# Performance work log

Measured on AMD Instinct MI355X. Metric: run time of the kernel, lower is better.

## Reference

```python
import jax, jax.numpy as jnp
import numpy as np

D_MODEL, D_STATE, D_CONV, D_INNER, DT_RANK, K = 96, 16, 3, 192, 6, 4
B, H, W = 1, 64, 64


def setup_inputs() -> dict:
    key = jax.random.key(0)
    ks = jax.random.split(key, 10)
    x = jax.random.normal(ks[0], (B, H, W, D_MODEL), jnp.float32)
    in_proj_w = jax.random.normal(ks[1], (2 * D_INNER, D_MODEL), jnp.float32) * 0.02
    conv_w = jax.random.normal(ks[2], (D_INNER, 1, D_CONV, D_CONV), jnp.float32) * 0.1
    conv_b = jnp.zeros((D_INNER,), jnp.float32)
    x_proj_w = jax.random.normal(ks[3], (K, DT_RANK + 2 * D_STATE, D_INNER), jnp.float32) * 0.02
    dt_std = DT_RANK ** -0.5
    dt_w = jax.random.uniform(ks[4], (K, D_INNER, DT_RANK), jnp.float32, -dt_std, dt_std)
    # dt bias init: inv-softplus of dt ~ logUniform(1e-3, 1e-1)
    u = jax.random.uniform(ks[5], (K, D_INNER), jnp.float32)
    dt = jnp.exp(u * (np.log(0.1) - np.log(0.001)) + np.log(0.001)).clip(1e-4)
    dt_b = dt + jnp.log(-jnp.expm1(-dt))
    A_logs = jnp.log(jnp.broadcast_to(jnp.arange(1, D_STATE + 1, dtype=jnp.float32), (K * D_INNER, D_STATE)))
    Ds = jnp.ones((K * D_INNER,), jnp.float32)
    ln_g = jnp.ones((D_INNER,), jnp.float32)
    ln_b = jnp.zeros((D_INNER,), jnp.float32)
    out_proj_w = jax.random.normal(ks[6], (D_MODEL, D_INNER), jnp.float32) * 0.02
    return dict(x=x, in_proj_w=in_proj_w, conv_w=conv_w, conv_b=conv_b, x_proj_w=x_proj_w,
                dt_w=dt_w, dt_b=dt_b, A_logs=A_logs, Ds=Ds, ln_g=ln_g, ln_b=ln_b,
                out_proj_w=out_proj_w)


def _ss2d(x, in_proj_w, conv_w, conv_b, x_proj_w, dt_w, dt_b, A_logs, Ds, ln_g, ln_b, out_proj_w):
    b, h, w, c = x.shape
    L = h * w
    d = conv_w.shape[0]            # d_inner
    n = A_logs.shape[1]            # d_state
    r = dt_w.shape[2]              # dt_rank
    # in_proj + split
    xz = jnp.einsum('bhwc,ec->bhwe', x, in_proj_w)
    xx, z = xz[..., :d], xz[..., d:]
    # depthwise conv (NCHW) + SiLU
    xc = xx.transpose(0, 3, 1, 2)
    pad = (D_CONV - 1) // 2
    xc = jax.lax.conv_general_dilated(xc, conv_w, (1, 1), [(pad, pad), (pad, pad)],
                                      feature_group_count=d) + conv_b[None, :, None, None]
    xc = jax.nn.silu(xc)
    # 4 scan directions: HW, WH, and their reverses
    x_hw = xc.reshape(b, d, L)
    x_wh = xc.transpose(0, 1, 3, 2).reshape(b, d, L)
    xs = jnp.stack([x_hw, x_wh, x_hw[..., ::-1], x_wh[..., ::-1]], axis=1)  # (b,K,d,L)
    x_dbl = jnp.einsum('bkdl,kcd->bkcl', xs, x_proj_w)
    dts, Bs, Cs = x_dbl[:, :, :r], x_dbl[:, :, r:r + n], x_dbl[:, :, r + n:]
    dts = jnp.einsum('bkrl,kdr->bkdl', dts, dt_w)
    delta = jax.nn.softplus(dts + dt_b[None, :, :, None])        # (b,K,d,L)
    A = -jnp.exp(A_logs).reshape(K, d, n)
    # time-major scanned inputs
    dA = jnp.exp(jnp.einsum('bkdl,kdn->lbkdn', delta, A))        # (L,b,K,d,n)
    dBu = jnp.einsum('bkdl,bknl,bkdl->lbkdn', delta, Bs, xs)
    Ct = Cs.transpose(3, 0, 1, 2)                                # (L,b,K,n)
    def step(hst, inp):
        dA_t, dBu_t, C_t = inp
        hst = dA_t * hst + dBu_t
        return hst, jnp.einsum('bkdn,bkn->bkd', hst, C_t)
    h0 = jnp.zeros((b, K, d, n), jnp.float32)
    _, ys = jax.lax.scan(step, h0, (dA, dBu, Ct))                # ys: (L,b,K,d)
    out_y = ys.transpose(1, 2, 3, 0) + xs * Ds.reshape(K, d)[None, :, :, None]
    # recombine directions
    inv = out_y[:, 2:4][..., ::-1]
    y1 = out_y[:, 0]
    y2 = inv[:, 0]
    wh = out_y[:, 1].reshape(b, d, w, h).transpose(0, 1, 3, 2).reshape(b, d, L)
    invwh = inv[:, 1].reshape(b, d, w, h).transpose(0, 1, 3, 2).reshape(b, d, L)
    y = (y1 + y2 + wh + invwh).transpose(0, 2, 1).reshape(b, h, w, d)
    # LayerNorm (eps=1e-5, torch default)
    mu = y.mean(-1, keepdims=True)
    var = ((y - mu) ** 2).mean(-1, keepdims=True)
    y = (y - mu) * jax.lax.rsqrt(var + 1e-5) * ln_g + ln_b
    y = y * jax.nn.silu(z)
    return jnp.einsum('bhwd,cd->bhwc', y, out_proj_w)


def reference(x, in_proj_w, conv_w, conv_b, x_proj_w, dt_w, dt_b, A_logs, Ds, ln_g, ln_b, out_proj_w):
    return _ss2d(x, in_proj_w, conv_w, conv_b, x_proj_w, dt_w, dt_b, A_logs, Ds, ln_g, ln_b, out_proj_w)
```

## Files before the change

### kernel.cpp

```cpp
#include <hip/hip_runtime.h>
#include <hip/hip_bf16.h>

#define LL 4096
#define DM 96
#define DI 192
#define NS 16
#define RK 6
#define RKP 8
#define KD 4
#define CPROJ 38
#define NC (KD*DI*NS)
#define PT 32
#define WS 196
#define OT 16
#define L2E 1.44269504f

__device__ __forceinline__ float b2f(__hip_bfloat16 v){ return __bfloat162float(v); }

__device__ __forceinline__ int detect_bf16(const unsigned short* __restrict__ xh, int tid, int* sflag){
  if (tid < 64){
    unsigned short u = xh[2*tid];
    int e = (u >> 7) & 0xFF;
    int sane = (e >= 107 && e <= 131) ? 1 : 0;
    unsigned long long m = __ballot(sane);
    if (tid == 0) *sflag = (__popcll(m) >= 32) ? 1 : 0;
  }
  return 0;
}

struct P12 { const void* p[12]; };
__global__ void k_convert_all(P12 ptrs, float* __restrict__ dst) {
  const int off[12] = {0,36864,38592,38784,67968,72576,73344,85632,86400,86592,86784,105216};
  __shared__ int sflag;
  detect_bf16((const unsigned short*)ptrs.p[0], threadIdx.x, &sflag);
  __syncthreads();
  int f = sflag;
  int i = blockIdx.x * 256 + threadIdx.x;
  if (i >= 105216) return;
  int j = 0;
  #pragma unroll
  for (int s = 1; s < 11; s++) if (i >= off[s]) j = s;
  int e = i - off[j];
  const void* src = ptrs.p[j+1];
  if (f) dst[i] = b2f(((const __hip_bfloat16*)src)[e]);
  else   dst[i] = ((const float*)src)[e];
}

__global__ void k_inproj(const void* __restrict__ xraw,
                         const float* __restrict__ w,
                         float* __restrict__ xx, float* __restrict__ z) {
  __shared__ float xr[8*DM];
  __shared__ int sflag;
  int tid = threadIdx.x;
  detect_bf16((const unsigned short*)xraw, tid, &sflag);
  __syncthreads();
  int l0 = blockIdx.x * 8;
  if (sflag){
    const __hip_bfloat16* xb = (const __hip_bfloat16*)xraw + (size_t)l0*DM;
    for (int i = tid; i < 8*DM; i += 384) xr[i] = b2f(xb[i]);
  } else {
    const float* xf = (const float*)xraw + (size_t)l0*DM;
    for (int i = tid; i < 8*DM; i += 384) xr[i] = xf[i];
  }
  __syncthreads();
  int e = tid;
  float acc[8];
  #pragma unroll
  for (int i=0;i<8;i++) acc[i]=0.f;
  const float* wr = w + e*DM;
  for (int c=0;c<DM;c++){
    float wv = wr[c];
    #pragma unroll
    for (int i=0;i<8;i++) acc[i] = fmaf(wv, xr[i*DM+c], acc[i]);
  }
  if (e < DI) {
    #pragma unroll
    for (int i=0;i<8;i++) xx[(l0+i)*DI + e] = acc[i];
  } else {
    int e2 = e - DI;
    #pragma unroll
    for (int i=0;i<8;i++) z[(l0+i)*DI + e2] = acc[i];
  }
}

__global__ void k_conv(const float* __restrict__ xx,
                       const float* __restrict__ cw,
                       const float* __restrict__ cb,
                       float* __restrict__ xc,
                       float* __restrict__ xct) {
  int l = blockIdx.x;
  int d = threadIdx.x;
  int h = l >> 6, w = l & 63;
  float acc = cb[d];
  #pragma unroll
  for (int ki=0; ki<3; ki++){
    int hh = h + ki - 1;
    if ((unsigned)hh >= 64u) continue;
    #pragma unroll
    for (int kj=0;kj<3;kj++){
      int wj = w + kj - 1;
      if ((unsigned)wj >= 64u) continue;
      acc = fmaf(cw[d*9 + ki*3 + kj], xx[(hh*64+wj)*DI + d], acc);
    }
  }
  float v = acc / (1.f + __expf(-acc));
  xc[l*DI + d] = v;
  xct[(((w<<6)|h))*DI + d] = v;
}

__device__ __forceinline__ int dir_map(int k, int t){
  if (k==0) return t;
  if (k==1) return ((t&63)<<6) | (t>>6);
  if (k==2) return 4095 - t;
  int u = 4095 - t; return ((u&63)<<6) | (u>>6);
}

__global__ void __launch_bounds__(256) k_proj(const float* __restrict__ xc,
                       const float* __restrict__ xpw,
                       float* __restrict__ dts,
                       float* __restrict__ Bb, float* __restrict__ Cb) {
  __shared__ float wl[CPROJ*WS];
  __shared__ float xs[PT*WS];
  int b = blockIdx.x;
  int k = b >> 7;
  int t_base = (b & 127) * PT;
  int tid = threadIdx.x;
  for (int idx = tid; idx < CPROJ*DI; idx += 256){
    int cc = idx / DI, j = idx - cc*DI;
    wl[cc*WS + j] = xpw[(k*CPROJ + cc)*DI + j];
  }
  for (int idx = tid; idx < PT*DI; idx += 256){
    int tt = idx / DI, j = idx - tt*DI;
    xs[tt*WS + j] = xc[dir_map(k, t_base + tt)*DI + j];
  }
  __syncthreads();
  int tg = tid & 7;
  int ty = tid >> 3;
  int cc0 = ty;
  int has2 = (ty + 32 < CPROJ);
  int cc1 = has2 ? (ty + 32) : ty;
  float a0x=0.f,a0y=0.f,a0z=0.f,a0w=0.f;
  float a1x=0.f,a1y=0.f,a1z=0.f,a1w=0.f;
  const float4* w0p = (const float4*)&wl[cc0*WS];
  const float4* w1p = (const float4*)&wl[cc1*WS];
  const float4* x0p = (const float4*)&xs[(tg     )*WS];
  const float4* x1p = (const float4*)&xs[(tg +  8)*WS];
  const float4* x2p = (const float4*)&xs[(tg + 16)*WS];
  const float4* x3p = (const float4*)&xs[(tg + 24)*WS];
  #pragma unroll 4
  for (int jc = 0; jc < DI/4; jc++){
    float4 w0 = w0p[jc], w1 = w1p[jc];
    float4 x0 = x0p[jc], x1 = x1p[jc], x2 = x2p[jc], x3 = x3p[jc];
    a0x = fmaf(w0.x,x0.x,fmaf(w0.y,x0.y,fmaf(w0.z,x0.z,fmaf(w0.w,x0.w,a0x))));
    a0y = fmaf(w0.x,x1.x,fmaf(w0.y,x1.y,fmaf(w0.z,x1.z,fmaf(w0.w,x1.w,a0y))));
    a0z = fmaf(w0.x,x2.x,fmaf(w0.y,x2.y,fmaf(w0.z,x2.z,fmaf(w0.w,x2.w,a0z))));
    a0w = fmaf(w0.x,x3.x,fmaf(w0.y,x3.y,fmaf(w0.z,x3.z,fmaf(w0.w,x3.w,a0w))));
    a1x = fmaf(w1.x,x0.x,fmaf(w1.y,x0.y,fmaf(w1.z,x0.z,fmaf(w1.w,x0.w,a1x))));
    a1y = fmaf(w1.x,x1.x,fmaf(w1.y,x1.y,fmaf(w1.z,x1.z,fmaf(w1.w,x1.w,a1y))));
    a1z = fmaf(w1.x,x2.x,fmaf(w1.y,x2.y,fmaf(w1.z,x2.z,fmaf(w1.w,x2.w,a1z))));
    a1w = fmaf(w1.x,x3.x,fmaf(w1.y,x3.y,fmaf(w1.z,x3.z,fmaf(w1.w,x3.w,a1w))));
  }
  float accs0[4] = {a0x,a0y,a0z,a0w};
  float accs1[4] = {a1x,a1y,a1z,a1w};
  #pragma unroll
  for (int i=0;i<4;i++){
    int t = t_base + tg + 8*i;
    size_t kt = (size_t)k*LL + t;
    {
      int cc = cc0; float v = accs0[i];
      if (cc < RK)            dts[kt*RKP + cc] = v;
      else if (cc < RK+NS)    Bb [kt*NS + (cc-RK)] = v;
      else                    Cb [kt*NS + (cc-RK-NS)] = v;
    }
    if (has2){
      int cc = ty + 32; float v = accs1[i];
      if (cc < RK+NS)         Bb [kt*NS + (cc-RK)] = v;
      else                    Cb [kt*NS + (cc-RK-NS)] = v;
    }
  }
}

template<int CHB>
__global__ void __launch_bounds__(256) k_scan1(
                      const float* __restrict__ xc_hw,
                      const float* __restrict__ xc_wh,
                      const float* __restrict__ dts,
                      const float* __restrict__ Bbuf,
                      const float* __restrict__ Cbuf,
                      const float* __restrict__ A_logs,
                      const float* __restrict__ dtw,
                      const float* __restrict__ dtb,
                      float* __restrict__ Pb, float* __restrict__ Hb,
                      float* __restrict__ SDb,
                      float* __restrict__ ydir) {
  constexpr int CS = LL >> CHB;
  int b = blockIdx.x;
  int c = b & ((1<<CHB)-1);
  int kg = b >> CHB;
  int k = kg / 3, dg3 = kg - k*3;
  int tid = threadIdx.x;
  int dl = tid >> 2, nq = tid & 3;
  int d = dg3*64 + dl;
  int kd = k*DI + d;
  float4 Al = *(const float4*)&A_logs[kd*NS + nq*4];
  float A0 = -__expf(Al.x)*L2E, A1 = -__expf(Al.y)*L2E;
  float A2 = -__expf(Al.z)*L2E, A3 = -__expf(Al.w)*L2E;
  float bt = dtb[kd];
  float w0 = dtw[kd*RK+0], w1 = dtw[kd*RK+1], w2 = dtw[kd*RK+2];
  float w3 = dtw[kd*RK+3], w4 = dtw[kd*RK+4], w5 = dtw[kd*RK+5];
  const float* dr = dts + ((size_t)k*LL + c*CS)*RKP;
  const float4* bp = (const float4*)(Bbuf + ((size_t)k*LL + c*CS)*NS) + nq;
  const float4* cp = (const float4*)(Cbuf + ((size_t)k*LL + c*CS)*NS) + nq;
  const float* xbase = (k & 1) ? xc_wh : xc_hw;
  int l0 = (k < 2) ? (c*CS) : (4095 - c*CS);
  int lstep = (k < 2) ? DI : -DI;
  const float* xp = xbase + (size_t)l0*DI + d;
  float* yp = ydir + ((size_t)k*LL + c*CS)*DI + d;
  float* sdp = SDb + ((size_t)k*LL + c*CS)*DI + d;
  float h0=0.f,h1=0.f,h2=0.f,h3=0.f, cumD=0.f;
  #pragma unroll
  for (int s=0; s<CS; s++){
    float4 lo = *(const float4*)(dr + s*RKP);
    float4 hi = *(const float4*)(dr + s*RKP + 4);
    float v = bt;
    v = fmaf(w0, lo.x, v); v = fmaf(w1, lo.y, v); v = fmaf(w2, lo.z, v);
    v = fmaf(w3, lo.w, v); v = fmaf(w4, hi.x, v); v = fmaf(w5, hi.y, v);
    float sp = (v > 20.f) ? v : __logf(1.f + __expf(v));
    cumD += sp;
    float sx = sp * xp[(ptrdiff_t)s*lstep];
    float4 bv = bp[s*4];
    float4 cv = cp[s*4];
    float a;
    a = exp2f(sp*A0); h0 = fmaf(a, h0, sx*bv.x);
    a = exp2f(sp*A1); h1 = fmaf(a, h1, sx*bv.y);
    a = exp2f(sp*A2); h2 = fmaf(a, h2, sx*bv.z);
    a = exp2f(sp*A3); h3 = fmaf(a, h3, sx*bv.w);
    float y = h0*cv.x + h1*cv.y + h2*cv.z + h3*cv.w;
    y += __shfl_xor(y, 1, 64);
    y += __shfl_xor(y, 2, 64);
    if (nq == 0){
      yp[s*DI] = y;
      sdp[s*DI] = cumD;
    }
  }
  int base = c*NC + kd*NS + nq*4;
  *(float4*)&Pb[base] = make_float4(exp2f(A0*cumD), exp2f(A1*cumD),
                                    exp2f(A2*cumD), exp2f(A3*cumD));
  *(float4*)&Hb[base] = make_float4(h0,h1,h2,h3);
}

template<int CHB>
__global__ void __launch_bounds__(256) k_scan2(
                      const float* __restrict__ Pb, float* __restrict__ Hb) {
  constexpr int CH = 1 << CHB;
  int idx = blockIdx.x*256 + threadIdx.x;
  float h = 0.f;
  #pragma unroll 8
  for (int c=0;c<CH;c++){
    float P = Pb[c*NC + idx];
    float Hc = Hb[c*NC + idx];
    Hb[c*NC + idx] = h;
    h = fmaf(P, h, Hc);
  }
}

template<int CHB>
__global__ void __launch_bounds__(192) k_corr(
                      const float* __restrict__ Cbuf,
                      const float* __restrict__ A_logs,
                      const float* __restrict__ Hb,
                      const float* __restrict__ SDb,
                      float* __restrict__ ydir) {
  constexpr int CS = LL >> CHB;
  int b = blockIdx.x;
  int k = b >> CHB;
  int c = b & ((1<<CHB)-1);
  if (c == 0) return;
  int t0 = c*CS;
  int d = threadIdx.x;
  int kd = k*DI + d;
  __shared__ float cs[CS*NS];
  for (int i = d; i < CS*NS; i += 192)
    cs[i] = Cbuf[((size_t)k*LL + t0)*NS + i];
  float A2[16], he[16];
  {
    const float4* ap = (const float4*)&A_logs[kd*NS];
    const float4* hp = (const float4*)&Hb[c*NC + kd*NS];
    #pragma unroll
    for (int i=0;i<4;i++){
      float4 av = ap[i];
      A2[4*i+0] = -__expf(av.x)*L2E; A2[4*i+1] = -__expf(av.y)*L2E;
      A2[4*i+2] = -__expf(av.z)*L2E; A2[4*i+3] = -__expf(av.w)*L2E;
      *(float4*)&he[4*i] = hp[i];
    }
  }
  __syncthreads();
  float* yp = ydir + ((size_t)k*LL + t0)*DI + d;
  const float* sdp = SDb + ((size_t)k*LL + t0)*DI + d;
  #pragma unroll 4
  for (int s=0; s<CS; s++){
    float SD = sdp[s*DI];
    float corr = 0.f;
    #pragma unroll
    for (int n=0;n<16;n++)
      corr = fmaf(cs[s*NS+n]*exp2f(A2[n]*SD), he[n], corr);
    yp[s*DI] += corr;
  }
}

__global__ void k_ln(const float* __restrict__ ydir,
                     const float* __restrict__ xc,
                     const float* __restrict__ z,
                     const float* __restrict__ Ds,
                     const float* __restrict__ ln_g,
                     const float* __restrict__ ln_b,
                     float* __restrict__ g) {
  int l = blockIdx.x;
  int d = threadIdx.x;
  int lt = ((l & 63) << 6) | (l >> 6);
  float y = ydir[(size_t)l*DI + d]
          + ydir[((size_t)LL   + lt)*DI + d]
          + ydir[((size_t)2*LL + (4095 - l))*DI + d]
          + ydir[((size_t)3*LL + (4095 - lt))*DI + d];
  float dsum = Ds[0*DI+d] + Ds[1*DI+d] + Ds[2*DI+d] + Ds[3*DI+d];
  y = fmaf(xc[l*DI+d], dsum, y);
  float s1 = y, s2 = y*y;
  #pragma unroll
  for (int off=32; off; off>>=1){
    s1 += __shfl_xor(s1, off, 64);
    s2 += __shfl_xor(s2, off, 64);
  }
  __shared__ float red[6];
  int wave = d >> 6;
  if ((d & 63) == 0){ red[wave] = s1; red[3+wave] = s2; }
  __syncthreads();
  float sum = red[0]+red[1]+red[2];
  float sq  = red[3]+red[4]+red[5];
  float mu = sum * (1.f/192.f);
  float var = sq * (1.f/192.f) - mu*mu;
  float rstd = rsqrtf(var + 1e-5f);
  float yn = (y - mu) * rstd * ln_g[d] + ln_b[d];
  float zv = z[l*DI + d];
  g[(size_t)l*DI + d] = yn * (zv / (1.f + __expf(-zv)));
}

__global__ void __launch_bounds__(192) k_oproj(const float* __restrict__ g,
                      const float* __restrict__ opw,
                      void* __restrict__ out,
                      const unsigned short* __restrict__ xh) {
  __shared__ float gs[OT*WS];
  __shared__ int sflag;
  int tid = threadIdx.x;
  detect_bf16(xh, tid, &sflag);
  int l0 = blockIdx.x * OT;
  const float4* gsrc = (const float4*)(g + (size_t)l0*DI);
  for (int idx = tid; idx < OT*DI/4; idx += 192){
    int row = idx / 48, col = idx - row*48;
    float4 v = gsrc[idx];
    *(float4*)&gs[row*WS + col*4] = v;
  }
  __syncthreads();
  int half = tid / 96;
  int e = tid - half*96;
  int r0 = half*8;
  float acc[8];
  #pragma unroll
  for (int i=0;i<8;i++) acc[i] = 0.f;
  const float4* wrow = (const float4*)(opw + e*DI);
  #pragma unroll 4
  for (int jc = 0; jc < DI/4; jc++){
    float4 w = wrow[jc];
    #pragma unroll
    for (int i=0;i<8;i++){
      float4 gv = *(const float4*)&gs[(r0+i)*WS + jc*4];
      acc[i] = fmaf(w.x,gv.x,fmaf(w.y,gv.y,fmaf(w.z,gv.z,fmaf(w.w,gv.w,acc[i]))));
    }
  }
  int f = sflag;
  #pragma unroll
  for (int i=0;i<8;i++){
    int l = l0 + r0 + i;
    if (f) ((__hip_bfloat16*)out)[l*DM + e] = __float2bfloat16(acc[i]);
    else   ((float*)out)[l*DM + e] = acc[i];
  }
}

extern "C" void kernel_launch(void* const* d_in, const int* in_sizes, int n_in,
                              void* d_out, int out_size, void* d_ws, size_t ws_size,
                              hipStream_t stream) {
  float* ws = (float*)d_ws;
  float* cvt = ws + 16;
  const int off[12] = {0,36864,38592,38784,67968,72576,73344,85632,86400,86592,86784,105216};
  float* c[12];
  c[0] = nullptr;
  for (int i = 1; i < 12; i++) c[i] = cvt + off[i-1];

  float* big    = cvt + 105216;
  float* xx     = big;
  float* z      = xx + (size_t)LL*DI;
  float* xc     = z  + (size_t)LL*DI;
  float* xct    = xc + (size_t)LL*DI;
  float* dts    = xct + (size_t)LL*DI;
  float* Bb     = dts + (size_t)KD*LL*RKP;
  float* Cb     = Bb + (size_t)KD*LL*NS;
  float* Pb     = Cb + (size_t)KD*LL*NS;
  size_t need256 = (size_t)(16 + 105216 + 4*786432 + 131072 + 2*262144
                            + 2*256*NC + 2*(size_t)KD*LL*DI) * 4;
  int chBits = (ws_size >= need256) ? 8 : 6;
  int CHn = 1 << chBits;
  float* Hb   = Pb + (size_t)CHn*NC;
  float* SDb  = Hb + (size_t)CHn*NC;
  float* ydir = SDb + (size_t)KD*LL*DI;
  float* g    = Pb;

  P12 ptrs;
  for (int i = 0; i < 12; i++) ptrs.p[i] = d_in[i];
  k_convert_all<<<(105216 + 255)/256, 256, 0, stream>>>(ptrs, cvt);

  k_inproj<<<LL/8, 384, 0, stream>>>(d_in[0], c[1], xx, z);
  k_conv<<<LL, DI, 0, stream>>>(xx, c[2], c[3], xc, xct);
  k_proj<<<KD*(LL/PT), 256, 0, stream>>>(xc, c[4], dts, Bb, Cb);
  if (chBits == 8){
    k_scan1<8><<<KD*3*256, 256, 0, stream>>>(xc, xct, dts, Bb, Cb, c[7], c[5], c[6],
                                             Pb, Hb, SDb, ydir);
    k_scan2<8><<<NC/256, 256, 0, stream>>>(Pb, Hb);
    k_corr<8><<<KD*256, 192, 0, stream>>>(Cb, c[7], Hb, SDb, ydir);
  } else {
    k_scan1<6><<<KD*3*64, 256, 0, stream>>>(xc, xct, dts, Bb, Cb, c[7], c[5], c[6],
                                            Pb, Hb, SDb, ydir);
    k_scan2<6><<<NC/256, 256, 0, stream>>>(Pb, Hb);
    k_corr<6><<<KD*64, 192, 0, stream>>>(Cb, c[7], Hb, SDb, ydir);
  }
  k_ln<<<LL, DI, 0, stream>>>(ydir, xc, z, c[8], c[9], c[10], g);
  k_oproj<<<LL/OT, 192, 0, stream>>>(g, c[11], d_out, (const unsigned short*)d_in[0]);
}
```

Before: 209.4 us.

## Fuse LayerNorm into output projection, interleave scan carries, use 128 chunks

Merges the LayerNorm/gating kernel into the output projection kernel. Each block now sums the four direction outputs, normalizes its 16 rows in shared memory and projects them directly, so the intermediate g buffer is neither written nor read back and one launch goes away. The per-chunk decay and carry state are stored interleaved as float2, so the carry-propagation pass reads one stream instead of two. The chunk count drops from 256 to 128, which halves the carry-propagation length and the correction blocks but doubles the serial length of each chunk in the first scan.

After: 202.8 us. 3.2% less time.

```diff
diff --git a/kernel.cpp b/kernel.cpp
--- a/kernel.cpp
+++ b/kernel.cpp
@@ -190,7 +190,7 @@
                       const float* __restrict__ A_logs,
                       const float* __restrict__ dtw,
                       const float* __restrict__ dtb,
-                      float* __restrict__ Pb, float* __restrict__ Hb,
+                      float* __restrict__ PH,
                       float* __restrict__ SDb,
                       float* __restrict__ ydir) {
   constexpr int CS = LL >> CHB;
@@ -243,24 +243,21 @@
       sdp[s*DI] = cumD;
     }
   }
-  int base = c*NC + kd*NS + nq*4;
-  *(float4*)&Pb[base] = make_float4(exp2f(A0*cumD), exp2f(A1*cumD),
-                                    exp2f(A2*cumD), exp2f(A3*cumD));
-  *(float4*)&Hb[base] = make_float4(h0,h1,h2,h3);
+  size_t base2 = ((size_t)c*NC + kd*NS + nq*4)*2;
+  *(float4*)&PH[base2]   = make_float4(exp2f(A0*cumD), h0, exp2f(A1*cumD), h1);
+  *(float4*)&PH[base2+4] = make_float4(exp2f(A2*cumD), h2, exp2f(A3*cumD), h3);
 }
 
 template<int CHB>
-__global__ void __launch_bounds__(256) k_scan2(
-                      const float* __restrict__ Pb, float* __restrict__ Hb) {
+__global__ void __launch_bounds__(256) k_scan2(float2* __restrict__ PH) {
   constexpr int CH = 1 << CHB;
   int idx = blockIdx.x*256 + threadIdx.x;
   float h = 0.f;
   #pragma unroll 8
   for (int c=0;c<CH;c++){
-    float P = Pb[c*NC + idx];
-    float Hc = Hb[c*NC + idx];
-    Hb[c*NC + idx] = h;
-    h = fmaf(P, h, Hc);
+    float2 ph = PH[(size_t)c*NC + idx];
+    PH[(size_t)c*NC + idx].y = h;
+    h = fmaf(ph.x, h, ph.y);
   }
 }
 
@@ -268,7 +265,7 @@
 __global__ void __launch_bounds__(192) k_corr(
                       const float* __restrict__ Cbuf,
                       const float* __restrict__ A_logs,
-                      const float* __restrict__ Hb,
+                      const float2* __restrict__ PH,
                       const float* __restrict__ SDb,
                       float* __restrict__ ydir) {
   constexpr int CS = LL >> CHB;
@@ -285,14 +282,15 @@
   float A2[16], he[16];
   {
     const float4* ap = (const float4*)&A_logs[kd*NS];
-    const float4* hp = (const float4*)&Hb[c*NC + kd*NS];
+    const float2* hp = PH + (size_t)c*NC + kd*NS;
     #pragma unroll
     for (int i=0;i<4;i++){
       float4 av = ap[i];
       A2[4*i+0] = -__expf(av.x)*L2E; A2[4*i+1] = -__expf(av.y)*L2E;
       A2[4*i+2] = -__expf(av.z)*L2E; A2[4*i+3] = -__expf(av.w)*L2E;
-      *(float4*)&he[4*i] = hp[i];
-    }
+    }
+    #pragma unroll
+    for (int n=0;n<16;n++) he[n] = hp[n].y;
   }
   __syncthreads();
   float* yp = ydir + ((size_t)k*LL + t0)*DI + d;
@@ -308,56 +306,61 @@
   }
 }
 
-__global__ void k_ln(const float* __restrict__ ydir,
-                     const float* __restrict__ xc,
-                     const float* __restrict__ z,
-                     const float* __restrict__ Ds,
-                     const float* __restrict__ ln_g,
-                     const float* __restrict__ ln_b,
-                     float* __restrict__ g) {
-  int l = blockIdx.x;
-  int d = threadIdx.x;
-  int lt = ((l & 63) << 6) | (l >> 6);
-  float y = ydir[(size_t)l*DI + d]
-          + ydir[((size_t)LL   + lt)*DI + d]
-          + ydir[((size_t)2*LL + (4095 - l))*DI + d]
-          + ydir[((size_t)3*LL + (4095 - lt))*DI + d];
-  float dsum = Ds[0*DI+d] + Ds[1*DI+d] + Ds[2*DI+d] + Ds[3*DI+d];
-  y = fmaf(xc[l*DI+d], dsum, y);
-  float s1 = y, s2 = y*y;
-  #pragma unroll
-  for (int off=32; off; off>>=1){
-    s1 += __shfl_xor(s1, off, 64);
-    s2 += __shfl_xor(s2, off, 64);
-  }
-  __shared__ float red[6];
-  int wave = d >> 6;
-  if ((d & 63) == 0){ red[wave] = s1; red[3+wave] = s2; }
-  __syncthreads();
-  float sum = red[0]+red[1]+red[2];
-  float sq  = red[3]+red[4]+red[5];
-  float mu = sum * (1.f/192.f);
-  float var = sq * (1.f/192.f) - mu*mu;
-  float rstd = rsqrtf(var + 1e-5f);
-  float yn = (y - mu) * rstd * ln_g[d] + ln_b[d];
-  float zv = z[l*DI + d];
-  g[(size_t)l*DI + d] = yn * (zv / (1.f + __expf(-zv)));
-}
-
-__global__ void __launch_bounds__(192) k_oproj(const float* __restrict__ g,
+__global__ void __launch_bounds__(192) k_out(
+                      const float* __restrict__ ydir,
+                      const float* __restrict__ xc,
+                      const float* __restrict__ z,
+                      const float* __restrict__ Ds,
+                      const float* __restrict__ ln_g,
+                      const float* __restrict__ ln_b,
                       const float* __restrict__ opw,
                       void* __restrict__ out,
                       const unsigned short* __restrict__ xh) {
   __shared__ float gs[OT*WS];
+  __shared__ float ps[2][OT][12];
+  __shared__ float mv[2][OT];
   __shared__ int sflag;
   int tid = threadIdx.x;
+  int d = tid;
   detect_bf16(xh, tid, &sflag);
   int l0 = blockIdx.x * OT;
-  const float4* gsrc = (const float4*)(g + (size_t)l0*DI);
-  for (int idx = tid; idx < OT*DI/4; idx += 192){
-    int row = idx / 48, col = idx - row*48;
-    float4 v = gsrc[idx];
-    *(float4*)&gs[row*WS + col*4] = v;
+  float dsum = Ds[d] + Ds[DI+d] + Ds[2*DI+d] + Ds[3*DI+d];
+  #pragma unroll 4
+  for (int r=0;r<OT;r++){
+    int l = l0 + r;
+    int lt = ((l & 63) << 6) | (l >> 6);
+    float y = ydir[(size_t)l*DI + d]
+            + ydir[((size_t)LL   + lt)*DI + d]
+            + ydir[((size_t)2*LL + (4095 - l))*DI + d]
+            + ydir[((size_t)3*LL + (4095 - lt))*DI + d];
+    gs[r*WS + d] = fmaf(xc[(size_t)l*DI + d], dsum, y);
+  }
+  __syncthreads();
+  {
+    int r = tid / 12, lane = tid - r*12;
+    float s1 = 0.f, s2 = 0.f;
+    for (int j = lane; j < DI; j += 12){
+      float v = gs[r*WS + j];
+      s1 += v; s2 += v*v;
+    }
+    ps[0][r][lane] = s1; ps[1][r][lane] = s2;
+  }
+  __syncthreads();
+  if (tid < OT){
+    float a = 0.f, bb = 0.f;
+    #pragma unroll
+    for (int j=0;j<12;j++){ a += ps[0][tid][j]; bb += ps[1][tid][j]; }
+    float mu = a * (1.f/192.f);
+    float var = bb * (1.f/192.f) - mu*mu;
+    mv[0][tid] = mu; mv[1][tid] = rsqrtf(var + 1e-5f);
+  }
+  __syncthreads();
+  float lg = ln_g[d], lb = ln_b[d];
+  #pragma unroll 4
+  for (int r=0;r<OT;r++){
+    float yn = (gs[r*WS + d] - mv[0][r]) * mv[1][r] * lg + lb;
+    float zv = z[(size_t)(l0+r)*DI + d];
+    gs[r*WS + d] = yn * (zv / (1.f + __expf(-zv)));
   }
   __syncthreads();
   int half = tid / 96;
@@ -403,15 +406,13 @@
   float* dts    = xct + (size_t)LL*DI;
   float* Bb     = dts + (size_t)KD*LL*RKP;
   float* Cb     = Bb + (size_t)KD*LL*NS;
-  float* Pb     = Cb + (size_t)KD*LL*NS;
-  size_t need256 = (size_t)(16 + 105216 + 4*786432 + 131072 + 2*262144
-                            + 2*256*NC + 2*(size_t)KD*LL*DI) * 4;
-  int chBits = (ws_size >= need256) ? 8 : 6;
+  float* PH     = Cb + (size_t)KD*LL*NS;
+  size_t need128 = (size_t)(16 + 105216 + 4*786432 + 131072 + 2*262144
+                            + 2*128*NC + 2*(size_t)KD*LL*DI) * 4;
+  int chBits = (ws_size >= need128) ? 7 : 6;
   int CHn = 1 << chBits;
-  float* Hb   = Pb + (size_t)CHn*NC;
-  float* SDb  = Hb + (size_t)CHn*NC;
+  float* SDb  = PH + 2*(size_t)CHn*NC;
   float* ydir = SDb + (size_t)KD*LL*DI;
-  float* g    = Pb;
 
   P12 ptrs;
   for (int i = 0; i < 12; i++) ptrs.p[i] = d_in[i];
@@ -420,17 +421,17 @@
   k_inproj<<<LL/8, 384, 0, stream>>>(d_in[0], c[1], xx, z);
   k_conv<<<LL, DI, 0, stream>>>(xx, c[2], c[3], xc, xct);
   k_proj<<<KD*(LL/PT), 256, 0, stream>>>(xc, c[4], dts, Bb, Cb);
-  if (chBits == 8){
-    k_scan1<8><<<KD*3*256, 256, 0, stream>>>(xc, xct, dts, Bb, Cb, c[7], c[5], c[6],
-                                             Pb, Hb, SDb, ydir);
-    k_scan2<8><<<NC/256, 256, 0, stream>>>(Pb, Hb);
-    k_corr<8><<<KD*256, 192, 0, stream>>>(Cb, c[7], Hb, SDb, ydir);
+  if (chBits == 7){
+    k_scan1<7><<<KD*3*128, 256, 0, stream>>>(xc, xct, dts, Bb, Cb, c[7], c[5], c[6],
+                                             PH, SDb, ydir);
+    k_scan2<7><<<NC/256, 256, 0, stream>>>((float2*)PH);
+    k_corr<7><<<KD*128, 192, 0, stream>>>(Cb, c[7], (const float2*)PH, SDb, ydir);
   } else {
     k_scan1<6><<<KD*3*64, 256, 0, stream>>>(xc, xct, dts, Bb, Cb, c[7], c[5], c[6],
-                                            Pb, Hb, SDb, ydir);
-    k_scan2<6><<<NC/256, 256, 0, stream>>>(Pb, Hb);
-    k_corr<6><<<KD*64, 192, 0, stream>>>(Cb, c[7], Hb, SDb, ydir);
-  }
-  k_ln<<<LL, DI, 0, stream>>>(ydir, xc, z, c[8], c[9], c[10], g);
-  k_oproj<<<LL/OT, 192, 0, stream>>>(g, c[11], d_out, (const unsigned short*)d_in[0]);
-}
+                                            PH, SDb, ydir);
+    k_scan2<6><<<NC/256, 256, 0, stream>>>((float2*)PH);
+    k_corr<6><<<KD*64, 192, 0, stream>>>(Cb, c[7], (const float2*)PH, SDb, ydir);
+  }
+  k_out<<<LL/OT, 192, 0, stream>>>(ydir, xc, z, c[8], c[9], c[10], c[11], d_out,
+                                   (const unsigned short*)d_in[0]);
+}
```
